# Kernel tuning notes

Hardware: AMD Instinct MI355X
Metric: run time of the kernel (lower is better)

The kernel has to match this reference:

```python
import jax, jax.numpy as jnp
import numpy as np

K = 512  # number of clusters
D = 128  # feature dim
N = 8192 # number of points


def setup_inputs() -> dict:
    key = jax.random.key(0)
    k1, k2 = jax.random.split(key)
    locF = jax.random.normal(k1, (N, 1, D), dtype=jnp.float32)
    Ck = jax.random.normal(k2, (1, K, D), dtype=jnp.float32)
    return {"locF": locF, "Ck": Ck}


def reference(locF, Ck):
    # locF: [N, 1, D], Ck: [1, K, D]
    x = locF[:, 0, :]          # [N, D]
    c = Ck[0]                  # [K, D]
    # (GEMM expansion avoids the [N, K, D] broadcast; argmin is unchanged)
    d2 = ((x * x).sum(-1, keepdims=True)
          - 2.0 * (x @ c.T)
          + (c * c).sum(-1)[None, :]) / D   # [N, K]
    index = jnp.argmin(d2, axis=1)           # [N]
    # per-cluster scatter-sum and counts (fused, single pass)
    Ck1 = jax.ops.segment_sum(x, index, num_segments=K)[None]  # [1, K, D]
    nItems = jax.ops.segment_sum(jnp.ones((x.shape[0],), dtype=jnp.int32),
                                 index, num_segments=K).reshape(1, -1)  # [1, K]
    return (Ck1, nItems)
```

## Files before the change

kernel.cpp:

```cpp
#include <hip/hip_runtime.h>
#include <hip/hip_bf16.h>

#define KC 512
#define DD 128
#define NP 8192


__global__ __launch_bounds__(256) void kprep(const float* __restrict__ Ck,
                                             float* __restrict__ CkT,
                                             float* __restrict__ sumc2,
                                             float* __restrict__ out) {
    const int b = blockIdx.x;
    const int t = threadIdx.x;
    if (b < 64) {
        const float4 v = *(const float4*)(Ck + b * 1024 + t * 4);
        const int k = b * 8 + (t >> 5);
        const int d = (t & 31) * 4;
        CkT[(d + 0) * KC + k] = v.x;
        CkT[(d + 1) * KC + k] = v.y;
        CkT[(d + 2) * KC + k] = v.z;
        CkT[(d + 3) * KC + k] = v.w;
    } else if (b == 64) {
        #pragma unroll
        for (int c = 0; c < 2; ++c) {
            const int k = t + c * 256;
            const float4* row = (const float4*)(Ck + k * DD);
            float s = 0.f;
            #pragma unroll
            for (int i = 0; i < 32; ++i) {
                const float4 v = row[i];
                s += v.x * v.x + v.y * v.y + v.z * v.z + v.w * v.w;
            }
            sumc2[k] = s;
        }
    } else {
        const int base = (b - 65) * 2048 + t;
        #pragma unroll
        for (int i = 0; i < 8; ++i) {
            const int idx = base + i * 256;
            if (idx < KC * DD + KC) out[idx] = 0.f;
        }
    }
}

__global__ __launch_bounds__(128) void kmain(const float* __restrict__ X,
                                             const float* __restrict__ CkT,
                                             const float* __restrict__ sumc2,
                                             float* __restrict__ out) {
    __shared__ __align__(16) float xs[8 * DD];
    __shared__ float bvx[2][8];
    __shared__ int   bix[2][8];
    __shared__ int   win[8];

    const int tid  = threadIdx.x;
    const int lane = tid & 63;
    const int h    = tid >> 6;
    const int p0   = blockIdx.x * 8;

    {
        const float4* Xv = (const float4*)(X + p0 * DD);
        float4* xv = (float4*)xs;
        xv[tid]       = Xv[tid];
        xv[tid + 128] = Xv[tid + 128];
    }
    __syncthreads();

    const float* cp = CkT + h * 256 + 4 * lane;

    float4 cn[4], cc[4];
    #pragma unroll
    for (int dd = 0; dd < 4; ++dd) cn[dd] = *(const float4*)(cp + dd * KC);

    float acc[8][4];
    #pragma unroll
    for (int p = 0; p < 8; ++p)
        #pragma unroll
        for (int j = 0; j < 4; ++j) acc[p][j] = 0.f;

    #pragma unroll 4
    for (int t = 0; t < 32; ++t) {
        #pragma unroll
        for (int dd = 0; dd < 4; ++dd) cc[dd] = cn[dd];
        if (t < 31) {
            #pragma unroll
            for (int dd = 0; dd < 4; ++dd)
                cn[dd] = *(const float4*)(cp + ((t + 1) * 4 + dd) * KC);
        }
        float4 xf[8];
        #pragma unroll
        for (int p = 0; p < 8; ++p)
            xf[p] = *(const float4*)&xs[p * DD + t * 4];
        #pragma unroll
        for (int dd = 0; dd < 4; ++dd) {
            #pragma unroll
            for (int p = 0; p < 8; ++p) {
                const float xv = (&xf[p].x)[dd];
                acc[p][0] = fmaf(xv, cc[dd].x, acc[p][0]);
                acc[p][1] = fmaf(xv, cc[dd].y, acc[p][1]);
                acc[p][2] = fmaf(xv, cc[dd].z, acc[p][2]);
                acc[p][3] = fmaf(xv, cc[dd].w, acc[p][3]);
            }
        }
    }

    float bestv[8];
    int   besti[8];
    #pragma unroll
    for (int p = 0; p < 8; ++p) { bestv[p] = 3.4e38f; besti[p] = 0; }
    const float4 s2v = *(const float4*)(sumc2 + h * 256 + 4 * lane);
    #pragma unroll
    for (int j = 0; j < 4; ++j) {
        const int cent = h * 256 + 4 * lane + j;
        const float s2 = (&s2v.x)[j];
        #pragma unroll
        for (int p = 0; p < 8; ++p) {
            const float v = fmaf(-2.f, acc[p][j], s2);
            if (v < bestv[p]) { bestv[p] = v; besti[p] = cent; }
        }
    }
    #pragma unroll
    for (int off = 1; off < 64; off <<= 1) {
        #pragma unroll
        for (int p = 0; p < 8; ++p) {
            const float ov = __shfl_xor(bestv[p], off);
            const int   oi = __shfl_xor(besti[p], off);
            if (ov < bestv[p] || (ov == bestv[p] && oi < besti[p])) {
                bestv[p] = ov; besti[p] = oi;
            }
        }
    }
    if (lane == 0) {
        #pragma unroll
        for (int p = 0; p < 8; ++p) { bvx[h][p] = bestv[p]; bix[h][p] = besti[p]; }
    }
    __syncthreads();
    if (tid < 8) {
        const float v0 = bvx[0][tid], v1 = bvx[1][tid];
        win[tid] = (v1 < v0) ? bix[1][tid] : bix[0][tid];
    }
    __syncthreads();

    #pragma unroll
    for (int i = 0; i < 8; ++i) {
        const int flat = tid + 128 * i;
        const int p = flat >> 7;
        const int d = flat & 127;
        atomicAdd(&out[win[p] * DD + d], xs[flat]);
    }
    if (tid < 8) atomicAdd(&out[KC * DD + win[tid]], 1.0f);
}

extern "C" void kernel_launch(void* const* d_in, const int* in_sizes, int n_in,
                              void* d_out, int out_size, void* d_ws, size_t ws_size,
                              hipStream_t stream) {
    const float* locF = (const float*)d_in[0];
    const float* Ck   = (const float*)d_in[1];
    float* out   = (float*)d_out;
    float* sumc2 = (float*)d_ws;
    float* CkT   = (float*)((char*)d_ws + 4096);

    hipLaunchKernelGGL(kprep, dim3(98), dim3(256), 0, stream, Ck, CkT, sumc2, out);
    hipLaunchKernelGGL(kmain, dim3(1024), dim3(128), 0, stream, locF, CkT, sumc2, out);
}
```

Measured before the change: 41.59 us.

## Replace global atomic scatter with LDS partial histograms and a reduction pass

The fused assign-and-scatter kernel is split into four stages: prep, assignment, per-group LDS histograms, and a final reduction. The assignment kernel now writes cluster indices plus per-slot integer counts, spread across 64 slots per cluster. A histogram kernel accumulates 128-point groups into shared-memory partial sums and writes them to a partial buffer, which a reduce kernel sums per cluster. The aim is to remove heavy contention from global float atomics on the output, at the cost of two extra launches and writing and re-reading a partial buffer of several megabytes.

```diff
diff --git a/kernel.cpp b/kernel.cpp
--- a/kernel.cpp
+++ b/kernel.cpp
@@ -9,7 +9,7 @@
 __global__ __launch_bounds__(256) void kprep(const float* __restrict__ Ck,
                                              float* __restrict__ CkT,
                                              float* __restrict__ sumc2,
-                                             float* __restrict__ out) {
+                                             int* __restrict__ cnts2) {
     const int b = blockIdx.x;
     const int t = threadIdx.x;
     if (b < 64) {
@@ -34,23 +34,20 @@
             sumc2[k] = s;
         }
     } else {
-        const int base = (b - 65) * 2048 + t;
-        #pragma unroll
-        for (int i = 0; i < 8; ++i) {
-            const int idx = base + i * 256;
-            if (idx < KC * DD + KC) out[idx] = 0.f;
-        }
-    }
-}
-
-__global__ __launch_bounds__(128) void kmain(const float* __restrict__ X,
-                                             const float* __restrict__ CkT,
-                                             const float* __restrict__ sumc2,
-                                             float* __restrict__ out) {
+        int* dst = cnts2 + (b - 65) * 2048;
+        #pragma unroll
+        for (int i = 0; i < 8; ++i) dst[t + 256 * i] = 0;
+    }
+}
+
+__global__ __launch_bounds__(128) void kassign(const float* __restrict__ X,
+                                               const float* __restrict__ CkT,
+                                               const float* __restrict__ sumc2,
+                                               int* __restrict__ idxout,
+                                               int* __restrict__ cnts2) {
     __shared__ __align__(16) float xs[8 * DD];
     __shared__ float bvx[2][8];
     __shared__ int   bix[2][8];
-    __shared__ int   win[8];
 
     const int tid  = threadIdx.x;
     const int lane = tid & 63;
@@ -136,18 +133,73 @@
     __syncthreads();
     if (tid < 8) {
         const float v0 = bvx[0][tid], v1 = bvx[1][tid];
-        win[tid] = (v1 < v0) ? bix[1][tid] : bix[0][tid];
-    }
-    __syncthreads();
-
-    #pragma unroll
-    for (int i = 0; i < 8; ++i) {
-        const int flat = tid + 128 * i;
-        const int p = flat >> 7;
-        const int d = flat & 127;
-        atomicAdd(&out[win[p] * DD + d], xs[flat]);
-    }
-    if (tid < 8) atomicAdd(&out[KC * DD + win[tid]], 1.0f);
+        const int c = (v1 < v0) ? bix[1][tid] : bix[0][tid];
+        idxout[p0 + tid] = c;
+        atomicAdd(&cnts2[c * 64 + (blockIdx.x & 63)], 1);
+    }
+}
+
+__global__ __launch_bounds__(256) void khist(const float* __restrict__ X,
+                                             const int* __restrict__ idx,
+                                             float* __restrict__ part) {
+    __shared__ float lds[256 * 64];
+    __shared__ int sidx[128];
+    const int b = blockIdx.x;
+    const int g = b >> 2, h = (b >> 1) & 1, ch = b & 1;
+    const int t = threadIdx.x;
+    const int lane = t & 63;
+    const int w = t >> 6;
+
+    {
+        float4* lz = (float4*)lds;
+        const float4 z = make_float4(0.f, 0.f, 0.f, 0.f);
+        #pragma unroll
+        for (int i = 0; i < 16; ++i) lz[t + 256 * i] = z;
+    }
+    if (t < 128) sidx[t] = idx[g * 128 + t];
+    __syncthreads();
+
+    const int clo = ch * 256;
+    const float* Xh = X + (size_t)g * 128 * DD + h * 64 + lane;
+    #pragma unroll 4
+    for (int i = 0; i < 32; ++i) {
+        const int p = w * 32 + i;
+        const int cl = sidx[p] - clo;
+        if ((unsigned)cl < 256u) {
+            const float x = Xh[p * DD];
+            atomicAdd(&lds[cl * 64 + lane], x);
+        }
+    }
+    __syncthreads();
+
+    const float4* ls = (const float4*)lds;
+    float* pg = part + (size_t)g * (KC * DD);
+    #pragma unroll
+    for (int r = 0; r < 16; ++r) {
+        const int j  = r * 256 + t;
+        const int cl = j >> 4;
+        const int dq = j & 15;
+        *(float4*)&pg[(clo + cl) * DD + h * 64 + dq * 4] = ls[j];
+    }
+}
+
+__global__ __launch_bounds__(128) void kreduce2(const float* __restrict__ part,
+                                                const int* __restrict__ cnts2,
+                                                float* __restrict__ out) {
+    const int c = blockIdx.x;
+    const int d = threadIdx.x;
+    const float* pc = part + (size_t)c * DD + d;
+    float s = 0.f;
+    #pragma unroll 8
+    for (int g = 0; g < 64; ++g) s += pc[(size_t)g * (KC * DD)];
+    out[c * DD + d] = s;
+
+    if (d < 64) {
+        int v = cnts2[c * 64 + d];
+        #pragma unroll
+        for (int off = 32; off > 0; off >>= 1) v += __shfl_xor(v, off);
+        if (d == 0) out[KC * DD + c] = (float)v;
+    }
 }
 
 extern "C" void kernel_launch(void* const* d_in, const int* in_sizes, int n_in,
@@ -156,9 +208,15 @@
     const float* locF = (const float*)d_in[0];
     const float* Ck   = (const float*)d_in[1];
     float* out   = (float*)d_out;
-    float* sumc2 = (float*)d_ws;
-    float* CkT   = (float*)((char*)d_ws + 4096);
-
-    hipLaunchKernelGGL(kprep, dim3(98), dim3(256), 0, stream, Ck, CkT, sumc2, out);
-    hipLaunchKernelGGL(kmain, dim3(1024), dim3(128), 0, stream, locF, CkT, sumc2, out);
-}
+    char*  ws    = (char*)d_ws;
+    float* sumc2 = (float*)(ws);
+    float* CkT   = (float*)(ws + 4096);
+    int*   idx   = (int*)(ws + 266240);
+    int*   cnts2 = (int*)(ws + 299008);
+    float* part  = (float*)(ws + 430080);
+
+    hipLaunchKernelGGL(kprep,    dim3(81),   dim3(256), 0, stream, Ck, CkT, sumc2, cnts2);
+    hipLaunchKernelGGL(kassign,  dim3(1024), dim3(128), 0, stream, locF, CkT, sumc2, idx, cnts2);
+    hipLaunchKernelGGL(khist,    dim3(256),  dim3(256), 0, stream, locF, idx, part);
+    hipLaunchKernelGGL(kreduce2, dim3(512),  dim3(128), 0, stream, part, cnts2, out);
+}
```

Result: slower. 56.86 us (+36.7%).
